# Optimization experiments

Hardware: AMD Instinct MI355X
Metric: run time of the kernel (lower is better)

The kernel has to match this reference:

```python
import jax, jax.numpy as jnp
import numpy as np

B, H, W, A = 8, 96, 96, 9
K_PRE = 4000          # pre-NMS top-k candidates
MAX_OUT = 2000        # max_output_size
IOU_T = 0.7           # iou_threshold
SCORE_T = 0.5         # hard score threshold from propose_score_bbox_pair
NEG = -1e9


def _make_anchors():
    # 3 scales x 3 aspect ratios on a HxW grid, normalized coords, (xmin,xmax,ymin,ymax)
    cy = (np.arange(H, dtype=np.float32) + 0.5) / H
    cx = (np.arange(W, dtype=np.float32) + 0.5) / W
    scales = np.array([0.05, 0.1, 0.2], dtype=np.float32)
    ratios = np.array([0.5, 1.0, 2.0], dtype=np.float32)
    ws = (scales[:, None] * np.sqrt(ratios)[None, :]).reshape(-1)  # [9]
    hs = (scales[:, None] / np.sqrt(ratios)[None, :]).reshape(-1)  # [9]
    cxg = cx[None, :, None]
    cyg = cy[:, None, None]
    xmin = np.broadcast_to(cxg - ws / 2, (H, W, A))
    xmax = np.broadcast_to(cxg + ws / 2, (H, W, A))
    ymin = np.broadcast_to(cyg - hs / 2, (H, W, A))
    ymax = np.broadcast_to(cyg + hs / 2, (H, W, A))
    return jnp.asarray(np.stack([xmin, xmax, ymin, ymax], axis=-1))  # [H,W,A,4]


def setup_inputs() -> dict:
    key = jax.random.key(0)
    k1, k2 = jax.random.split(key)
    score_map = jax.random.uniform(k1, (B, H, W, A), dtype=jnp.float32)
    delta_map = jax.random.normal(k2, (B, H, W, A * 4), dtype=jnp.float32) * 0.2
    anchors = _make_anchors()
    return {"score_map": score_map, "delta_map": delta_map, "anchors": anchors}


def _decode(delta_map, anchors):
    # delta_map: [B,H,W,4A] -> [B,H,W,A,4]; anchors: [H,W,A,4] (xmin,xmax,ymin,ymax)
    d = delta_map.reshape(B, H, W, A, 4)
    tx, ty, tw, th = d[..., 0], d[..., 1], d[..., 2], d[..., 3]
    xa = (anchors[..., 0] + anchors[..., 1]) * 0.5
    ya = (anchors[..., 2] + anchors[..., 3]) * 0.5
    wa = anchors[..., 1] - anchors[..., 0]
    ha = anchors[..., 3] - anchors[..., 2]
    x = tx * wa + xa
    y = ty * ha + ya
    w = jnp.exp(tw) * wa
    h = jnp.exp(th) * ha
    boxes = jnp.stack([x - w / 2, x + w / 2, y - h / 2, y + h / 2], axis=-1)
    return jnp.clip(boxes, 0.0, 1.0)  # trim_bboxes / manual clipping


def _pairwise_iou(b):
    # b: [K,4] (xmin,xmax,ymin,ymax)
    xmin, xmax, ymin, ymax = b[:, 0], b[:, 1], b[:, 2], b[:, 3]
    area = (xmax - xmin) * (ymax - ymin)
    iw = jnp.maximum(jnp.minimum(xmax[:, None], xmax[None, :])
                     - jnp.maximum(xmin[:, None], xmin[None, :]), 0.0)
    ih = jnp.maximum(jnp.minimum(ymax[:, None], ymax[None, :])
                     - jnp.maximum(ymin[:, None], ymin[None, :]), 0.0)
    inter = iw * ih
    union = area[:, None] + area[None, :] - inter
    return inter / jnp.maximum(union, 1e-8)


def _nms_single(boxes, scores):
    # boxes: [N,4], scores: [N]. Hard NMS (soft_nms_sigma=0).
    masked = jnp.where(scores > SCORE_T, scores, NEG)  # score threshold
    vals, idx = jax.lax.top_k(masked, K_PRE)           # pre-NMS top-k
    cand = boxes[idx]                                  # [K_PRE,4]
    iou = _pairwise_iou(cand)                          # [K_PRE,K_PRE]
    ar = jnp.arange(K_PRE)

    def step(s, _):
        i = jnp.argmax(s)
        ok = s[i] > NEG / 2
        sup = (iou[i] > IOU_T) | (ar == i)
        s = jnp.where(sup, NEG, s)
        return s, (i, ok)

    _, (sel, ok) = jax.lax.scan(step, vals, None, length=MAX_OUT)
    return jnp.where(ok[:, None], cand[sel], 0.0)      # [MAX_OUT,4], zero-padded


def reference(score_map, delta_map, anchors):
    boxes = _decode(delta_map, anchors).reshape(B, H * W * A, 4)
    scores = score_map.reshape(B, H * W * A)
    return jax.vmap(_nms_single)(boxes, scores)        # [B,MAX_OUT,4]
```

## Files before the change

### kernel.cpp

```cpp
#include <hip/hip_runtime.h>
#include <stdint.h>

#define NB 8
#define NH 96
#define NW_ 96
#define NA 9
#define NANCH (NH * NW_ * NA)
#define KPRE 4000
#define MAXOUT 2000
#define KEYCAP 4224
#define NWORDS 63
#define GTASKS 528
#define EB_CAP 2048
#define ELTOT 8192

typedef unsigned long long u64;

__device__ __forceinline__ u64 readlane64(u64 v, int l) {
    unsigned lo = (unsigned)__builtin_amdgcn_readlane((int)(unsigned)v, l);
    unsigned hi = (unsigned)__builtin_amdgcn_readlane((int)(unsigned)(v >> 32), l);
    return ((u64)hi << 32) | lo;
}
__device__ __forceinline__ float readlane_f(float v, int l) {
    return __uint_as_float((unsigned)__builtin_amdgcn_readlane((int)__float_as_uint(v), l));
}

__global__ __launch_bounds__(256) void k_hist(const float* __restrict__ score,
                                              unsigned* __restrict__ hist) {
    const int b = blockIdx.y;
    __shared__ unsigned h[4096];
    for (int i = threadIdx.x; i < 4096; i += 256) h[i] = 0u;
    __syncthreads();
    const float4* s4 = (const float4*)(score + (size_t)b * NANCH);
    int i0 = blockIdx.x * 256 + threadIdx.x;
    const int stride = 16 * 256;
    for (int i = i0; i < NANCH / 4; i += stride) {
        float4 v = s4[i];
        if (v.x > 0.5f) atomicAdd(&h[(__float_as_uint(v.x) >> 11) & 4095u], 1u);
        if (v.y > 0.5f) atomicAdd(&h[(__float_as_uint(v.y) >> 11) & 4095u], 1u);
        if (v.z > 0.5f) atomicAdd(&h[(__float_as_uint(v.z) >> 11) & 4095u], 1u);
        if (v.w > 0.5f) atomicAdd(&h[(__float_as_uint(v.w) >> 11) & 4095u], 1u);
    }
    __syncthreads();
    for (int k = threadIdx.x; k < 4096; k += 256) {
        unsigned c = h[k];
        if (c) atomicAdd(&hist[b * 4096 + k], c);
    }
}

__global__ __launch_bounds__(64) void k_cut(unsigned* __restrict__ hist,
                                            unsigned* __restrict__ start,
                                            unsigned* __restrict__ meta,
                                            unsigned* __restrict__ ecnt) {
    const int b = blockIdx.x;
    const int lane = threadIdx.x;
    const int base = b * 4096 + lane * 64;
    ecnt[b * 64 + lane] = 0u;
    unsigned v[64];
#pragma unroll
    for (int k = 0; k < 64; ++k) { v[k] = hist[base + k]; }
#pragma unroll
    for (int k = 0; k < 64; ++k) { hist[base + k] = 0u; }
#pragma unroll
    for (int k = 62; k >= 0; --k) v[k] += v[k + 1];
    unsigned tot = v[0];
    unsigned incl = tot;
#pragma unroll
    for (int d = 1; d < 64; d <<= 1) {
        unsigned t = __shfl_down(incl, d);
        if (lane + d < 64) incl += t;
    }
    unsigned sfx_above = incl - tot;
    unsigned total = __shfl(incl, 0);
#pragma unroll
    for (int k = 0; k < 63; ++k) start[base + k] = v[k + 1] + sfx_above;
    start[base + 63] = sfx_above;
    if (lane == 0) {
        unsigned P = total < KEYCAP ? total : KEYCAP;
        meta[b] = 0u;
        meta[8 + b] = P;
        meta[16 + b] = P < KPRE ? P : KPRE;
    }
#pragma unroll
    for (int k = 0; k < 64; ++k) {
        unsigned sfxk = v[k] + sfx_above;
        unsigned nxt = (k < 63) ? (v[k + 1] + sfx_above) : sfx_above;
        if (sfxk >= (unsigned)KPRE && nxt < (unsigned)KPRE) {
            unsigned P = sfxk < KEYCAP ? sfxk : KEYCAP;
            meta[b] = (unsigned)(lane * 64 + k);
            meta[8 + b] = P;
            meta[16 + b] = (unsigned)KPRE;
        }
    }
}

__global__ void k_collect(const float* __restrict__ score, const unsigned* __restrict__ meta,
                          const unsigned* __restrict__ start, unsigned* __restrict__ bcnt,
                          u64* __restrict__ keys) {
    const int b = blockIdx.y;
    const unsigned cut = meta[b];
    const float* sc = score + (size_t)b * NANCH;
    int i0 = blockIdx.x * blockDim.x + threadIdx.x;
    int stride = gridDim.x * blockDim.x;
    for (int i = i0; i < NANCH; i += stride) {
        float v = sc[i];
        if (v > 0.5f) {
            unsigned bits = __float_as_uint(v);
            unsigned bucket = (bits >> 11) & 4095u;
            if (bucket >= cut) {
                unsigned pos = start[b * 4096 + bucket] + atomicAdd(&bcnt[b * 4096 + bucket], 1u);
                if (pos < (unsigned)KEYCAP)
                    keys[(size_t)b * KEYCAP + pos] =
                        ((u64)bits << 32) | (unsigned)(~(unsigned)i);
            }
        }
    }
}

__global__ void k_rank_decode(const u64* __restrict__ keys,
                              const unsigned* __restrict__ start,
                              const unsigned* __restrict__ meta,
                              const float* __restrict__ delta,
                              const float* __restrict__ anchors,
                              float* __restrict__ cand) {
#pragma clang fp contract(off)
    const int b = blockIdx.y;
    const int s = blockIdx.x * blockDim.x + threadIdx.x;
    const int P = (int)meta[8 + b];
    const int M = (int)meta[16 + b];
    if (s >= M && s < KPRE) {
        float4* c4 = (float4*)(cand + (size_t)b * KPRE * 4);
        c4[s] = make_float4(0.f, 0.f, 0.f, 0.f);
    }
    if (s >= P) return;
    const u64* kb = keys + (size_t)b * KEYCAP;
    u64 key = kb[s];
    unsigned bucket = (unsigned)(key >> 43) & 4095u;
    int base = (int)start[b * 4096 + bucket];
    int end = (bucket > 0) ? (int)start[b * 4096 + bucket - 1] : P;
    if (end > P) end = P;
    int rank = 0;
    for (int t = base; t < end; ++t) rank += (kb[t] > key) ? 1 : 0;
    int pos = base + rank;
    if (pos >= KPRE) return;
    int n = (int)(~(unsigned)(key & 0xFFFFFFFFull));
    float4 t4 = *(const float4*)(delta + ((size_t)b * NANCH + n) * 4);
    float4 a4 = *(const float4*)(anchors + (size_t)n * 4);
    float xa = (a4.x + a4.y) * 0.5f;
    float ya = (a4.z + a4.w) * 0.5f;
    float wa = a4.y - a4.x;
    float ha = a4.w - a4.z;
    float x = t4.x * wa + xa;
    float y = t4.y * ha + ya;
    float w = expf(t4.z) * wa;
    float h = expf(t4.w) * ha;
    float xmn = fminf(fmaxf(x - w * 0.5f, 0.f), 1.f);
    float xmx = fminf(fmaxf(x + w * 0.5f, 0.f), 1.f);
    float ymn = fminf(fmaxf(y - h * 0.5f, 0.f), 1.f);
    float ymx = fminf(fmaxf(y + h * 0.5f, 0.f), 1.f);
    float* o = cand + ((size_t)b * KPRE + pos) * 4;
    o[0] = xmn; o[1] = xmx; o[2] = ymn; o[3] = ymx;
}

__global__ __launch_bounds__(256) void k_geo(const float* __restrict__ cand,
                                             unsigned* __restrict__ ecnt,
                                             unsigned* __restrict__ ebuf) {
#pragma clang fp contract(off)
    const int b = blockIdx.y;
    const int h = blockIdx.z;
    const int lane = threadIdx.x & 63;
    const int wv = threadIdx.x >> 6;
    int t = (blockIdx.x << 2) + wv;
    int c = 0;
    while (true) { int n = (NWORDS - c + 3) >> 2; if (t < n) break; t -= n; ++c; }
    const int wbase = c + (t << 2);
    const bool nd0 = (wbase != c);

    const float4* c4 = (const float4*)(cand + (size_t)b * KPRE * 4);
    const int iq0 = c << 6;
    const int il = iq0 + lane;
    float4 bi_l;
    float ai_l;
    if (il < KPRE) {
        bi_l = c4[il];
        ai_l = (bi_l.y - bi_l.x) * (bi_l.w - bi_l.z);
    } else {
        bi_l = make_float4(2.f, -1.f, 2.f, -1.f);
        ai_l = 0.f;
    }
    float ai69_l = 0.69f * ai_l;

    unsigned* cl = &ecnt[b * 64 + c];
    unsigned* bb = ebuf + ((size_t)(b * 64 + c)) * EB_CAP;

    float4 bq0, bq1, bq2, bq3;
    float aq0, aq1, aq2, aq3, aq69_0, aq69_1, aq69_2, aq69_3;
#define LOADQ(S)                                                              \
    { int w_ = wbase + S; int jq_ = (w_ << 6) + lane;                         \
      if (w_ < NWORDS && jq_ < KPRE) {                                        \
          bq##S = c4[jq_];                                                    \
          aq##S = (bq##S.y - bq##S.x) * (bq##S.w - bq##S.z);                  \
      } else { bq##S = make_float4(2.f, -1.f, 2.f, -1.f); aq##S = 0.f; }      \
      aq69_##S = 0.69f * aq##S; }
    LOADQ(0) LOADQ(1) LOADQ(2) LOADQ(3)
#undef LOADQ

#pragma unroll 4
    for (int ii = 0; ii < 32; ++ii) {
        const int i = (h << 5) | ii;
        float bix = readlane_f(bi_l.x, i);
        float biy = readlane_f(bi_l.y, i);
        float biz = readlane_f(bi_l.z, i);
        float biw = readlane_f(bi_l.w, i);
        float ai69 = readlane_f(ai69_l, i);
        bool ok0, ok1, ok2, ok3;
        float in0, in1, in2, in3;
#define PAIR(S, OKV, INV)                                                     \
        { float iw = fminf(biy, bq##S.y) - fmaxf(bix, bq##S.x);               \
          float ih = fminf(biw, bq##S.w) - fmaxf(biz, bq##S.z);               \
          iw = fmaxf(iw, 0.0f); ih = fmaxf(ih, 0.0f);                         \
          INV = iw * ih;                                                      \
          OKV = INV > fmaxf(ai69, aq69_##S); }
        PAIR(0, ok0, in0) PAIR(1, ok1, in1) PAIR(2, ok2, in2) PAIR(3, ok3, in3)
#undef PAIR
        ok0 = ok0 && (nd0 || lane > i);
        if (__any(ok0 | ok1 | ok2 | ok3)) {
            float ai = readlane_f(ai_l, i);
            u64 wd0 = 0, wd1 = 0, wd2 = 0, wd3 = 0;
#define HITS(S, OKV, INV, WD)                                                 \
            if (__any(OKV)) {                                                 \
                float uni = ai + aq##S - INV;                                 \
                WD = __ballot(OKV && (INV / fmaxf(uni, 1e-8f) > 0.7f));       \
            }
            HITS(0, ok0, in0, wd0) HITS(1, ok1, in1, wd1)
            HITS(2, ok2, in2, wd2) HITS(3, ok3, in3, wd3)
#undef HITS
            if (lane == 0) {
                int pc = __builtin_popcountll(wd0) + __builtin_popcountll(wd1) +
                         __builtin_popcountll(wd2) + __builtin_popcountll(wd3);
                if (pc) {
                    unsigned slot = atomicAdd(cl, (unsigned)pc);
                    unsigned ibase = (unsigned)(iq0 + i) << 12;
#define WR(S, WD)                                                             \
                    { u64 w_ = WD; unsigned jb = (unsigned)((wbase + S) << 6);\
                      while (w_) { int jj = __builtin_ctzll(w_);              \
                          w_ &= w_ - 1;                                       \
                          if (slot < (unsigned)EB_CAP)                        \
                              bb[slot] = ibase | (jb + (unsigned)jj);         \
                          ++slot; } }
                    WR(0, wd0) WR(1, wd1) WR(2, wd2) WR(3, wd3)
#undef WR
                }
            }
        }
    }
}

__global__ __launch_bounds__(256) void k_nms(const float* __restrict__ cand,
                                             const unsigned* __restrict__ ecnt,
                                             const unsigned* __restrict__ ebuf,
                                             const unsigned* __restrict__ meta,
                                             float* __restrict__ out) {
#pragma clang fp contract(off)
    const int b = blockIdx.x;
    const int tid = threadIdx.x;
    const int lane = tid & 63;
    const int wv = tid >> 6;
    const int M = (int)meta[16 + b];
    const int nchunks = (M + 63) >> 6;

    __shared__ u64 accS[64];
    __shared__ u64 supS[64];
    __shared__ unsigned offS[65];
    __shared__ unsigned eflat[ELTOT];
    __shared__ int sel[MAXOUT];
    __shared__ float4 bxF[KPRE];
    __shared__ float sarF[KPRE];
    __shared__ int s_cnt, s_fb, s_changed;

    if (tid == 0) { s_cnt = 0; s_fb = 0; }
    __syncthreads();
    if (wv == 0) {
        unsigned n = ecnt[b * 64 + lane];
        if (n > (unsigned)EB_CAP) atomicOr(&s_fb, 1);
        unsigned scan = n;
#pragma unroll
        for (int d = 1; d < 64; d <<= 1) {
            unsigned t = __shfl_up(scan, d);
            if (lane >= d) scan += t;
        }
        offS[lane + 1] = scan;
        if (lane == 0) offS[0] = 0u;
        if (lane == 63 && scan > (unsigned)ELTOT) atomicOr(&s_fb, 1);
    }
    if (tid < 64) {
        int lo = tid << 6;
        u64 vmask = 0ull;
        if (lo < M) {
            int nr = M - lo;
            vmask = (nr >= 64) ? ~0ull : ((1ull << nr) - 1ull);
        }
        accS[tid] = vmask;
    }
    __syncthreads();
    const bool fb = s_fb != 0;
    const unsigned E = offS[64];

    if (!fb) {
        {
            const int c = tid & 63;
            const int sub = tid >> 6;
            const unsigned o0 = offS[c];
            const unsigned n = offS[c + 1] - o0;
            const unsigned* bb = ebuf + ((size_t)(b * 64 + c)) * EB_CAP;
            for (unsigned e = (unsigned)sub; e < n; e += 4u)
                eflat[o0 + e] = bb[e];
        }
        __syncthreads();

        for (int pass = 0; pass < 8192; ++pass) {
            if (tid < 64) supS[tid] = 0ull;
            if (tid == 0) s_changed = 0;
            __syncthreads();
            for (unsigned e = (unsigned)tid; e < E; e += 256u) {
                unsigned ed = eflat[e];
                unsigned i = ed >> 12;
                unsigned j = ed & 4095u;
                if ((accS[i >> 6] >> (i & 63)) & 1ull)
                    atomicOr((unsigned*)&supS[j >> 6] + ((j >> 5) & 1u),
                             1u << (j & 31u));
            }
            __syncthreads();
            if (tid < 64) {
                int lo = tid << 6;
                u64 vmask = 0ull;
                if (lo < M) {
                    int nr = M - lo;
                    vmask = (nr >= 64) ? ~0ull : ((1ull << nr) - 1ull);
                }
                u64 na = vmask & ~supS[tid];
                if (na != accS[tid]) { accS[tid] = na; s_changed = 1; }
            }
            __syncthreads();
            if (s_changed == 0) break;
        }

        if (wv == 0) {
            u64 aw = accS[lane];
            int pc = __builtin_popcountll(aw);
            int scan = pc;
#pragma unroll
            for (int d = 1; d < 64; d <<= 1) {
                int t = __shfl_up(scan, d);
                if (lane >= d) scan += t;
            }
            int pos = scan - pc;
            int total = __shfl(scan, 63);
            int cnt = total < MAXOUT ? total : MAXOUT;
            int kept = MAXOUT - pos;
            kept = kept < 0 ? 0 : (kept > pc ? pc : kept);
            for (int t = 0; t < pc - kept; ++t)
                aw &= ~(0x8000000000000000ull >> __builtin_clzll(aw));
            while (aw) {
                int r = __builtin_ctzll(aw);
                aw &= aw - 1;
                sel[pos++] = (lane << 6) + r;
            }
            if (lane == 0) s_cnt = cnt;
        }
    } else {
        const float4* c4 = (const float4*)(cand + (size_t)b * KPRE * 4);
        for (int k = tid; k < KPRE; k += 256) {
            float4 v = c4[k];
            bxF[k] = v;
            sarF[k] = (v.y - v.x) * (v.w - v.z);
        }
        __syncthreads();
        if (wv == 0) {
            auto iougt = [&](float4 A, float aA, float4 Bq, float aB) -> bool {
#pragma clang fp contract(off)
                float iw = fminf(A.y, Bq.y) - fmaxf(A.x, Bq.x);
                iw = fmaxf(iw, 0.0f);
                float ih = fminf(A.w, Bq.w) - fmaxf(A.z, Bq.z);
                ih = fmaxf(ih, 0.0f);
                float inter = iw * ih;
                float uni = aA + aB - inter;
                return inter / fmaxf(uni, 1e-8f) > 0.7f;
            };
            u64 accReg = 0ull;
            int cnt = 0;
            for (int c = 0; c < nchunks && cnt < MAXOUT; ++c) {
                int r = (c << 6) + lane;
                bool valid = r < M;
                float4 bq = valid ? bxF[r] : make_float4(0.f, 0.f, 0.f, 0.f);
                float aq = valid ? sarF[r] : 0.f;
                u64 inT = 0ull;
                for (int i2 = 0; i2 < 64; ++i2) {
                    if (valid && i2 < lane) {
                        int ri = (c << 6) + i2;
                        if (iougt(bxF[ri], sarF[ri], bq, aq)) inT |= 1ull << i2;
                    }
                }
                bool supb = false;
                for (int cc = 0; cc < c; ++cc) {
                    u64 aw = readlane64(accReg, cc);
                    while (aw) {
                        int rb = __builtin_ctzll(aw);
                        aw &= aw - 1;
                        int ia = (cc << 6) + rb;
                        if (valid && iougt(bxF[ia], sarF[ia], bq, aq)) supb = true;
                    }
                }
                u64 live = __ballot(valid && !supb);
                u64 am = 0ull;
                while (live) {
                    u64 pred = __ballot((inT & live) != 0ull);
                    u64 acc = live & ~pred;
                    u64 sup = __ballot((inT & acc) != 0ull);
                    am |= acc;
                    live &= ~(acc | sup);
                }
                int pc = __builtin_popcountll(am);
                if (cnt + pc >= MAXOUT) {
                    int drop = cnt + pc - MAXOUT;
                    for (int t = 0; t < drop; ++t)
                        am &= ~(0x8000000000000000ull >> __builtin_clzll(am));
                    pc = MAXOUT - cnt;
                }
                if (lane == 0) {
                    u64 tmp = am;
                    int p = cnt;
                    while (tmp) {
                        int rr = __builtin_ctzll(tmp);
                        tmp &= tmp - 1;
                        sel[p++] = (c << 6) + rr;
                    }
                }
                if (lane == c) accReg |= am;
                cnt += pc;
            }
            if (lane == 0) s_cnt = cnt;
        }
    }
    __syncthreads();

    const int cntF = s_cnt;
    const float4* c4o = (const float4*)(cand + (size_t)b * KPRE * 4);
    float4* o4 = (float4*)(out + (size_t)b * MAXOUT * 4);
    for (int r = tid; r < MAXOUT; r += 256) {
        float4 v = make_float4(0.0f, 0.0f, 0.0f, 0.0f);
        if (r < cntF) v = c4o[sel[r]];
        o4[r] = v;
    }
}

extern "C" void kernel_launch(void* const* d_in, const int* in_sizes, int n_in,
                              void* d_out, int out_size, void* d_ws, size_t ws_size,
                              hipStream_t stream) {
    const float* score   = (const float*)d_in[0];
    const float* delta   = (const float*)d_in[1];
    const float* anchors = (const float*)d_in[2];
    float* out = (float*)d_out;

    uint8_t* w8 = (uint8_t*)d_ws;
    unsigned* hist  = (unsigned*)(w8 + 0);
    unsigned* start = (unsigned*)(w8 + 131072);
    unsigned* meta  = (unsigned*)(w8 + 262144);
    unsigned* ecnt  = (unsigned*)(w8 + 262272);
    u64* keys       = (u64*)(w8 + 264320);
    float* cand     = (float*)(w8 + 534656);
    unsigned* ebuf  = (unsigned*)(w8 + 1046656);

    hipMemsetAsync(hist, 0, 131072, stream);
    k_hist<<<dim3(16, NB), 256, 0, stream>>>(score, hist);
    k_cut<<<NB, 64, 0, stream>>>(hist, start, meta, ecnt);
    k_collect<<<dim3(32, NB), 256, 0, stream>>>(score, meta, start, hist , keys);
    k_rank_decode<<<dim3((KEYCAP + 255) / 256, NB), 256, 0, stream>>>(keys, start, meta,
                                                                      delta, anchors, cand);
    k_geo<<<dim3(GTASKS / 4, NB, 2), 256, 0, stream>>>(cand, ecnt, ebuf);
    k_nms<<<NB, 256, 0, stream>>>(cand, ecnt, ebuf, meta, out);
}
```

Measured before the change: 84.96 us.

## Drop memset and fuse rank-decode into collect via last-block pattern

Each histogram block now writes its own private histogram, and k_cut sums them. This removes the hipMemsetAsync and the global atomics, and k_cut now also zeroes the bucket counters. The rank/decode kernel is folded into k_collect: the last block to finish for each batch, detected with a threadfence and an atomic counter, ranks and decodes all keys, so one kernel launch disappears. In exchange, rank/decode work that used to run across 17 blocks per batch now runs in a single 256-thread block, which serialises it. k_cut also has to read 8 times as much histogram data.

```diff
diff --git a/kernel.cpp b/kernel.cpp
--- a/kernel.cpp
+++ b/kernel.cpp
@@ -13,6 +13,8 @@
 #define GTASKS 528
 #define EB_CAP 2048
 #define ELTOT 8192
+#define HBLK 8
+#define CBLK 32
 
 typedef unsigned long long u64;
 
@@ -26,14 +28,15 @@
 }
 
 __global__ __launch_bounds__(256) void k_hist(const float* __restrict__ score,
-                                              unsigned* __restrict__ hist) {
+                                              unsigned* __restrict__ phist) {
     const int b = blockIdx.y;
+    const int g = blockIdx.x;
     __shared__ unsigned h[4096];
     for (int i = threadIdx.x; i < 4096; i += 256) h[i] = 0u;
     __syncthreads();
     const float4* s4 = (const float4*)(score + (size_t)b * NANCH);
-    int i0 = blockIdx.x * 256 + threadIdx.x;
-    const int stride = 16 * 256;
+    int i0 = g * 256 + threadIdx.x;
+    const int stride = HBLK * 256;
     for (int i = i0; i < NANCH / 4; i += stride) {
         float4 v = s4[i];
         if (v.x > 0.5f) atomicAdd(&h[(__float_as_uint(v.x) >> 11) & 4095u], 1u);
@@ -42,25 +45,31 @@
         if (v.w > 0.5f) atomicAdd(&h[(__float_as_uint(v.w) >> 11) & 4095u], 1u);
     }
     __syncthreads();
-    for (int k = threadIdx.x; k < 4096; k += 256) {
-        unsigned c = h[k];
-        if (c) atomicAdd(&hist[b * 4096 + k], c);
-    }
-}
-
-__global__ __launch_bounds__(64) void k_cut(unsigned* __restrict__ hist,
+    unsigned* dst = phist + ((size_t)(b * HBLK + g) << 12);
+    for (int k = threadIdx.x; k < 4096; k += 256) dst[k] = h[k];
+}
+
+__global__ __launch_bounds__(64) void k_cut(const unsigned* __restrict__ phist,
                                             unsigned* __restrict__ start,
                                             unsigned* __restrict__ meta,
-                                            unsigned* __restrict__ ecnt) {
+                                            unsigned* __restrict__ ecnt,
+                                            unsigned* __restrict__ bcnt,
+                                            unsigned* __restrict__ dcnt) {
     const int b = blockIdx.x;
     const int lane = threadIdx.x;
     const int base = b * 4096 + lane * 64;
     ecnt[b * 64 + lane] = 0u;
+    if (lane == 0) dcnt[b] = 0u;
+#pragma unroll
+    for (int k = 0; k < 64; ++k) bcnt[base + k] = 0u;
     unsigned v[64];
 #pragma unroll
-    for (int k = 0; k < 64; ++k) { v[k] = hist[base + k]; }
-#pragma unroll
-    for (int k = 0; k < 64; ++k) { hist[base + k] = 0u; }
+    for (int k = 0; k < 64; ++k) v[k] = 0u;
+    for (int g = 0; g < HBLK; ++g) {
+        const unsigned* src = phist + ((size_t)(b * HBLK + g) << 12) + lane * 64;
+#pragma unroll
+        for (int k = 0; k < 64; ++k) v[k] += src[k];
+    }
 #pragma unroll
     for (int k = 62; k >= 0; --k) v[k] += v[k + 1];
     unsigned tot = v[0];
@@ -94,14 +103,21 @@
     }
 }
 
-__global__ void k_collect(const float* __restrict__ score, const unsigned* __restrict__ meta,
-                          const unsigned* __restrict__ start, unsigned* __restrict__ bcnt,
-                          u64* __restrict__ keys) {
+__global__ __launch_bounds__(256) void k_collect(const float* __restrict__ score,
+                                                 const unsigned* __restrict__ meta,
+                                                 const unsigned* __restrict__ start,
+                                                 unsigned* __restrict__ bcnt,
+                                                 u64* __restrict__ keys,
+                                                 const float* __restrict__ delta,
+                                                 const float* __restrict__ anchors,
+                                                 float* __restrict__ cand,
+                                                 unsigned* __restrict__ dcnt) {
+#pragma clang fp contract(off)
     const int b = blockIdx.y;
     const unsigned cut = meta[b];
     const float* sc = score + (size_t)b * NANCH;
-    int i0 = blockIdx.x * blockDim.x + threadIdx.x;
-    int stride = gridDim.x * blockDim.x;
+    int i0 = blockIdx.x * 256 + threadIdx.x;
+    const int stride = CBLK * 256;
     for (int i = i0; i < NANCH; i += stride) {
         float v = sc[i];
         if (v > 0.5f) {
@@ -115,51 +131,55 @@
             }
         }
     }
-}
-
-__global__ void k_rank_decode(const u64* __restrict__ keys,
-                              const unsigned* __restrict__ start,
-                              const unsigned* __restrict__ meta,
-                              const float* __restrict__ delta,
-                              const float* __restrict__ anchors,
-                              float* __restrict__ cand) {
-#pragma clang fp contract(off)
-    const int b = blockIdx.y;
-    const int s = blockIdx.x * blockDim.x + threadIdx.x;
+
+    __shared__ int s_last;
+    __threadfence();
+    if (threadIdx.x == 0) {
+        unsigned done = atomicAdd(&dcnt[b], 1u);
+        s_last = (done == (unsigned)(CBLK - 1)) ? 1 : 0;
+    }
+    __syncthreads();
+    if (!s_last) return;
+    __threadfence();
+
     const int P = (int)meta[8 + b];
     const int M = (int)meta[16 + b];
-    if (s >= M && s < KPRE) {
-        float4* c4 = (float4*)(cand + (size_t)b * KPRE * 4);
-        c4[s] = make_float4(0.f, 0.f, 0.f, 0.f);
-    }
-    if (s >= P) return;
     const u64* kb = keys + (size_t)b * KEYCAP;
-    u64 key = kb[s];
-    unsigned bucket = (unsigned)(key >> 43) & 4095u;
-    int base = (int)start[b * 4096 + bucket];
-    int end = (bucket > 0) ? (int)start[b * 4096 + bucket - 1] : P;
-    if (end > P) end = P;
-    int rank = 0;
-    for (int t = base; t < end; ++t) rank += (kb[t] > key) ? 1 : 0;
-    int pos = base + rank;
-    if (pos >= KPRE) return;
-    int n = (int)(~(unsigned)(key & 0xFFFFFFFFull));
-    float4 t4 = *(const float4*)(delta + ((size_t)b * NANCH + n) * 4);
-    float4 a4 = *(const float4*)(anchors + (size_t)n * 4);
-    float xa = (a4.x + a4.y) * 0.5f;
-    float ya = (a4.z + a4.w) * 0.5f;
-    float wa = a4.y - a4.x;
-    float ha = a4.w - a4.z;
-    float x = t4.x * wa + xa;
-    float y = t4.y * ha + ya;
-    float w = expf(t4.z) * wa;
-    float h = expf(t4.w) * ha;
-    float xmn = fminf(fmaxf(x - w * 0.5f, 0.f), 1.f);
-    float xmx = fminf(fmaxf(x + w * 0.5f, 0.f), 1.f);
-    float ymn = fminf(fmaxf(y - h * 0.5f, 0.f), 1.f);
-    float ymx = fminf(fmaxf(y + h * 0.5f, 0.f), 1.f);
-    float* o = cand + ((size_t)b * KPRE + pos) * 4;
-    o[0] = xmn; o[1] = xmx; o[2] = ymn; o[3] = ymx;
+    for (int s = threadIdx.x; s < KEYCAP; s += 256) {
+        if (s >= M && s < KPRE) {
+            float4* c4 = (float4*)(cand + (size_t)b * KPRE * 4);
+            c4[s] = make_float4(0.f, 0.f, 0.f, 0.f);
+        }
+        if (s < P) {
+            u64 key = kb[s];
+            unsigned bucket = (unsigned)(key >> 43) & 4095u;
+            int base = (int)start[b * 4096 + bucket];
+            int end = (bucket > 0) ? (int)start[b * 4096 + bucket - 1] : P;
+            if (end > P) end = P;
+            int rank = 0;
+            for (int t = base; t < end; ++t) rank += (kb[t] > key) ? 1 : 0;
+            int pos = base + rank;
+            if (pos < KPRE) {
+                int n = (int)(~(unsigned)(key & 0xFFFFFFFFull));
+                float4 t4 = *(const float4*)(delta + ((size_t)b * NANCH + n) * 4);
+                float4 a4 = *(const float4*)(anchors + (size_t)n * 4);
+                float xa = (a4.x + a4.y) * 0.5f;
+                float ya = (a4.z + a4.w) * 0.5f;
+                float wa = a4.y - a4.x;
+                float ha = a4.w - a4.z;
+                float x = t4.x * wa + xa;
+                float y = t4.y * ha + ya;
+                float w = expf(t4.z) * wa;
+                float h = expf(t4.w) * ha;
+                float xmn = fminf(fmaxf(x - w * 0.5f, 0.f), 1.f);
+                float xmx = fminf(fmaxf(x + w * 0.5f, 0.f), 1.f);
+                float ymn = fminf(fmaxf(y - h * 0.5f, 0.f), 1.f);
+                float ymx = fminf(fmaxf(y + h * 0.5f, 0.f), 1.f);
+                float* o = cand + ((size_t)b * KPRE + pos) * 4;
+                o[0] = xmn; o[1] = xmx; o[2] = ymn; o[3] = ymx;
+            }
+        }
+    }
 }
 
 __global__ __launch_bounds__(256) void k_geo(const float* __restrict__ cand,
@@ -463,20 +483,20 @@
     float* out = (float*)d_out;
 
     uint8_t* w8 = (uint8_t*)d_ws;
-    unsigned* hist  = (unsigned*)(w8 + 0);
-    unsigned* start = (unsigned*)(w8 + 131072);
-    unsigned* meta  = (unsigned*)(w8 + 262144);
-    unsigned* ecnt  = (unsigned*)(w8 + 262272);
-    u64* keys       = (u64*)(w8 + 264320);
-    float* cand     = (float*)(w8 + 534656);
-    unsigned* ebuf  = (unsigned*)(w8 + 1046656);
-
-    hipMemsetAsync(hist, 0, 131072, stream);
-    k_hist<<<dim3(16, NB), 256, 0, stream>>>(score, hist);
-    k_cut<<<NB, 64, 0, stream>>>(hist, start, meta, ecnt);
-    k_collect<<<dim3(32, NB), 256, 0, stream>>>(score, meta, start, hist , keys);
-    k_rank_decode<<<dim3((KEYCAP + 255) / 256, NB), 256, 0, stream>>>(keys, start, meta,
-                                                                      delta, anchors, cand);
+    unsigned* phist = (unsigned*)(w8 + 0);
+    unsigned* start = (unsigned*)(w8 + 1048576);
+    unsigned* bcnt  = (unsigned*)(w8 + 1179648);
+    unsigned* meta  = (unsigned*)(w8 + 1310720);
+    unsigned* ecnt  = (unsigned*)(w8 + 1310848);
+    unsigned* dcnt  = (unsigned*)(w8 + 1312896);
+    u64* keys       = (u64*)(w8 + 1312928);
+    float* cand     = (float*)(w8 + 1583264);
+    unsigned* ebuf  = (unsigned*)(w8 + 2095264);
+
+    k_hist<<<dim3(HBLK, NB), 256, 0, stream>>>(score, phist);
+    k_cut<<<NB, 64, 0, stream>>>(phist, start, meta, ecnt, bcnt, dcnt);
+    k_collect<<<dim3(CBLK, NB), 256, 0, stream>>>(score, meta, start, bcnt, keys,
+                                                  delta, anchors, cand, dcnt);
     k_geo<<<dim3(GTASKS / 4, NB, 2), 256, 0, stream>>>(cand, ecnt, ebuf);
     k_nms<<<NB, 256, 0, stream>>>(cand, ecnt, ebuf, meta, out);
 }
```

After: 148.7 us. 1.75x slower.
